# Kernel tuning notes

Hardware: AMD Instinct MI355X
Metric: run time of the kernel (lower is better)

## Reference

```python
import jax, jax.numpy as jnp
import numpy as np

N, E, D_IN, D_H, G = 20000, 320000, 512, 256, 128


def setup_inputs() -> dict:
    key = jax.random.key(0)
    ks = jax.random.split(key, 9)
    x = jax.random.normal(ks[0], (N, D_IN), dtype=jnp.float32)
    edge_index = jax.random.randint(ks[1], (2, E), 0, N, dtype=jnp.int32)
    batch = jnp.sort(jax.random.randint(ks[2], (N,), 0, G, dtype=jnp.int32))
    W1 = jax.random.normal(ks[3], (D_IN, D_H), dtype=jnp.float32) / np.float32(np.sqrt(D_IN))
    b1 = jnp.zeros((D_H,), dtype=jnp.float32)
    W2 = jax.random.normal(ks[4], (D_H, D_H), dtype=jnp.float32) / np.float32(np.sqrt(D_H))
    b2 = jnp.zeros((D_H,), dtype=jnp.float32)
    w_fc = jax.random.normal(ks[5], (D_H, 1), dtype=jnp.float32) / np.float32(np.sqrt(D_H))
    b_fc = jnp.zeros((1,), dtype=jnp.float32)
    return {"x": x, "edge_index": edge_index, "batch": batch,
            "W1": W1, "b1": b1, "W2": W2, "b2": b2, "w_fc": w_fc, "b_fc": b_fc}


def gcn_conv(x, W, b, src, dst, n):
    # PyG GCNConv: out = D^{-1/2} (A+I) D^{-1/2} (X W) + b  (self-loops already in src/dst)
    xw = x @ W                                            # [n, d_out]
    deg = jnp.zeros((n,), xw.dtype).at[dst].add(1.0)       # in-degree incl. self loop
    dinv = jnp.where(deg > 0, jax.lax.rsqrt(deg), 0.0)
    coef = (dinv[src] * dinv[dst])[:, None]               # [e, 1]
    out = jnp.zeros_like(xw).at[dst].add(xw[src] * coef)  # gather-scale-scatter
    return out + b


def reference(x, edge_index, batch, W1, b1, W2, b2, w_fc, b_fc):
    n = x.shape[0]
    loops = jnp.arange(n, dtype=edge_index.dtype)
    src = jnp.concatenate([edge_index[0], loops])
    dst = jnp.concatenate([edge_index[1], loops])
    h = jax.nn.relu(gcn_conv(x, W1, b1, src, dst, n))
    h = jax.nn.relu(gcn_conv(h, W2, b2, src, dst, n))
    # global_mean_pool over graph ids
    sums = jax.ops.segment_sum(h, batch, num_segments=G)                      # [G, d]
    cnt = jax.ops.segment_sum(jnp.ones((n, 1), h.dtype), batch, num_segments=G)
    pooled = sums / jnp.maximum(cnt, 1.0)
    return (pooled @ w_fc + b_fc)[:, 0]                                       # [G]
```

## Files before the change

kernel.cpp:

```cpp
#include <hip/hip_runtime.h>
#include <hip/hip_fp16.h>


#define TPB 256
#define CAP 64

typedef _Float16 hfrag __attribute__((ext_vector_type(8)));
typedef float f32x4 __attribute__((ext_vector_type(4)));
typedef float f32x2 __attribute__((ext_vector_type(2)));

__global__ __launch_bounds__(TPB) void k_init(int* __restrict__ cursor, int N,
                                              const float* __restrict__ W1,
                                              unsigned short* __restrict__ B1, int K1) {
  int nbz = (N + TPB - 1) / TPB;
  int b = blockIdx.x;
  if (b < nbz) {
    int i = b * TPB + threadIdx.x;
    if (i < N) cursor[i] = 0;
    return;
  }
  int t = (b - nbz) * TPB + threadIdx.x;
  if (t >= K1 * 256) return;
  int n = t & 255, k = t >> 8;
  __half h = __float2half(W1[(size_t)k * 256 + n]);
  B1[((size_t)(k >> 5) * 256 + n) * 32 + (k & 31)] = *(unsigned short*)&h;
}

#define LDSTR 72

template <int MODE>
__device__ __forceinline__ void gemm_core(const unsigned short* __restrict__ Bp,
                                          unsigned char* __restrict__ C, int M, int K,
                                          int bm, int bn,
                                          unsigned short (*As)[LDSTR],
                                          const float* A_f32,
                                          const __half* A_f16) {
  const int tid = threadIdx.x;
  const int w = tid >> 6;
  const int lane = tid & 63;
  const int q = lane >> 4;
  const int nin = lane & 15;
  const int r  = tid >> 3;
  const int cb = (tid & 7) << 3;
  const int row = bm + r;
  const bool rok = row < M;

  size_t bbase[2];
#pragma unroll
  for (int nt = 0; nt < 2; ++nt)
    bbase[nt] = ((size_t)(bn + w * 32 + nt * 16 + nin)) * 32 + q * 8;

  f32x4 acc[2][2];
#pragma unroll
  for (int mf = 0; mf < 2; ++mf)
#pragma unroll
    for (int nt = 0; nt < 2; ++nt) acc[mf][nt] = (f32x4){0.f, 0.f, 0.f, 0.f};

  float4 fA[2], fB[2];
  uint4  hA, hB;

  auto loadf = [&](float4* rf, int kb2) {
    const float* Ap = A_f32 + (size_t)row * K + kb2 + cb;
    rf[0] = *(const float4*)(Ap);
    rf[1] = *(const float4*)(Ap + 4);
  };
  auto loadh = [&](uint4& rh, int kb2) {
    rh = *(const uint4*)(A_f16 + (size_t)row * K + kb2 + cb);
  };
  auto stagef = [&](float4* rf) {
    float vv[8];
    *(float4*)&vv[0] = rf[0]; *(float4*)&vv[4] = rf[1];
    unsigned short h8[8];
#pragma unroll
    for (int j = 0; j < 8; ++j) {
      __half h = __float2half(vv[j]);
      h8[j] = *(unsigned short*)&h;
    }
    __syncthreads();
    *(uint4*)&As[r][cb] = *(uint4*)&h8[0];
    __syncthreads();
  };
  auto stageh = [&](uint4& rh) {
    __syncthreads();
    *(uint4*)&As[r][cb] = rh;
    __syncthreads();
  };
  auto mfma_step = [&](int kb2) {
#pragma unroll
    for (int s = 0; s < 2; ++s) {
      const size_t koff = (size_t)((kb2 >> 5) + s) * 256 * 32;
      hfrag bf[2];
#pragma unroll
      for (int nt = 0; nt < 2; ++nt)
        bf[nt] = *(const hfrag*)(Bp + koff + bbase[nt]);
      hfrag af[2];
#pragma unroll
      for (int mf = 0; mf < 2; ++mf)
        af[mf] = *(const hfrag*)&As[mf * 16 + nin][s * 32 + q * 8];
#pragma unroll
      for (int mf = 0; mf < 2; ++mf)
#pragma unroll
        for (int nt = 0; nt < 2; ++nt)
          acc[mf][nt] = __builtin_amdgcn_mfma_f32_16x16x32_f16(af[mf], bf[nt], acc[mf][nt], 0, 0, 0);
    }
  };

  if (MODE == 0) {
    fA[0] = make_float4(0.f, 0.f, 0.f, 0.f); fA[1] = fA[0];
    fB[0] = fA[0]; fB[1] = fA[0];
    if (rok) { loadf(fA, 0); loadf(fB, 64); }
  } else {
    hA = make_uint4(0, 0, 0, 0); hB = hA;
    if (rok) { loadh(hA, 0); loadh(hB, 64); }
  }

  for (int kb = 0; kb < K; kb += 128) {
    if (MODE == 0) stagef(fA); else stageh(hA);
    int kpA = kb + 128;
    if (kpA < K && rok) { if (MODE == 0) loadf(fA, kpA); else loadh(hA, kpA); }
    mfma_step(kb);
    if (MODE == 0) stagef(fB); else stageh(hB);
    int kpB = kb + 192;
    if (kpB < K && rok) { if (MODE == 0) loadf(fB, kpB); else loadh(hB, kpB); }
    mfma_step(kb + 64);
  }

#pragma unroll
  for (int mf = 0; mf < 2; ++mf) {
    int rb = bm + mf * 16 + q * 4;
#pragma unroll
    for (int reg = 0; reg < 4; ++reg) {
      int rr = rb + reg;
      if (rr < M) {
#pragma unroll
        for (int nt = 0; nt < 2; ++nt) {
          float v = acc[mf][nt][reg];
          int pk = __builtin_amdgcn_cvt_pk_fp8_f32(v, v, 0, false);
          C[(size_t)rr * 256 + bn + w * 32 + nt * 16 + nin] = (unsigned char)(pk & 0xff);
        }
      }
    }
  }
}

__global__ __launch_bounds__(TPB) void k_gemm1_scatter(const float* __restrict__ A,
                                                       const unsigned short* __restrict__ Bp,
                                                       unsigned char* __restrict__ C, int M, int K,
                                                       const int* __restrict__ src,
                                                       const int* __restrict__ dst,
                                                       int* __restrict__ cursor,
                                                       unsigned* __restrict__ pairw, int E,
                                                       const float* __restrict__ W2,
                                                       unsigned short* __restrict__ W2h) {
  __shared__ unsigned short As[32][LDSTR];
  int nbg = 2 * ((M + 31) / 32);
  int b = blockIdx.x;
  if (b < nbg) {
    gemm_core<0>(Bp, C, M, K, (b >> 1) * 32, (b & 1) * 128, As, A, nullptr);
    return;
  }
  b -= nbg;
  int nbE = (E + TPB - 1) / TPB;
  if (b < nbE) {
    int e = b * TPB + threadIdx.x;
    if (e >= E) return;
    int s = src[e], d = dst[e];
    int pos = d * CAP + atomicAdd(&cursor[d], 1);
    pairw[pos] = (unsigned)s;
    return;
  }
  b -= nbE;
  int t = b * TPB + threadIdx.x;
  if (t >= 256 * 256) return;
  int n = t & 255, k = t >> 8;
  __half h = __float2half(W2[(size_t)k * 256 + n]);
  W2h[((size_t)(k >> 5) * 256 + n) * 32 + (k & 31)] = *(unsigned short*)&h;
}

__global__ __launch_bounds__(TPB) void k_gemm2(const __half* __restrict__ A,
                                               const unsigned short* __restrict__ Bp,
                                               unsigned char* __restrict__ C, int M, int K) {
  __shared__ unsigned short As[32][LDSTR];
  gemm_core<1>(Bp, C, M, K, blockIdx.y * 32, blockIdx.x * 128, As, nullptr, A);
}

__device__ __forceinline__ void fma16(float* a, float coef, uint4 v) {
#pragma unroll
  for (int wv = 0; wv < 4; ++wv) {
    unsigned word = (&v.x)[wv];
    f32x2 lo = __builtin_amdgcn_cvt_pk_f32_fp8((int)word, false);
    f32x2 hi = __builtin_amdgcn_cvt_pk_f32_fp8((int)word, true);
    a[4 * wv + 0] = fmaf(coef, lo[0], a[4 * wv + 0]);
    a[4 * wv + 1] = fmaf(coef, lo[1], a[4 * wv + 1]);
    a[4 * wv + 2] = fmaf(coef, hi[0], a[4 * wv + 2]);
    a[4 * wv + 3] = fmaf(coef, hi[1], a[4 * wv + 3]);
  }
}

__device__ __forceinline__ void gather_loop(float* a, const uint4* __restrict__ xq,
                                            unsigned wreg, int deg, int quarter, int li) {
  int iters = (deg + 3) >> 2;
  int itersP = (iters + 3) & ~3;
  for (int p = 0; p < itersP; p += 4) {
    int k0 = 4 * p + quarter;
    unsigned w0 = (unsigned)__shfl((int)wreg, k0);
    unsigned w1 = (unsigned)__shfl((int)wreg, k0 + 4);
    unsigned w2 = (unsigned)__shfl((int)wreg, k0 + 8);
    unsigned w3 = (unsigned)__shfl((int)wreg, k0 + 12);
    uint4 v0 = xq[((size_t)(w0 >> 16) << 4) + li];
    uint4 v1 = xq[((size_t)(w1 >> 16) << 4) + li];
    uint4 v2 = xq[((size_t)(w2 >> 16) << 4) + li];
    uint4 v3 = xq[((size_t)(w3 >> 16) << 4) + li];
    unsigned short c0 = (unsigned short)(w0 & 0xFFFFu);
    unsigned short c1 = (unsigned short)(w1 & 0xFFFFu);
    unsigned short c2 = (unsigned short)(w2 & 0xFFFFu);
    unsigned short c3 = (unsigned short)(w3 & 0xFFFFu);
    fma16(a, __half2float(*(__half*)&c0), v0);
    fma16(a, __half2float(*(__half*)&c1), v1);
    fma16(a, __half2float(*(__half*)&c2), v2);
    fma16(a, __half2float(*(__half*)&c3), v3);
  }
#pragma unroll
  for (int i = 0; i < 16; ++i) a[i] += __shfl_xor(a[i], 16);
#pragma unroll
  for (int i = 0; i < 16; ++i) a[i] += __shfl_xor(a[i], 32);
}

__global__ __launch_bounds__(TPB) void k_gather1(const uint4* __restrict__ xq,
                                                 const int* __restrict__ cnt,
                                                 unsigned* __restrict__ pairw,
                                                 const float* __restrict__ bias,
                                                 uint4* __restrict__ h1, int N) {
  int node = __builtin_amdgcn_readfirstlane(blockIdx.x * 4 + (threadIdx.x >> 6));
  if (node >= N) return;
  int deg = __builtin_amdgcn_readfirstlane(cnt[node]);
  int lane = threadIdx.x & 63;
  int quarter = lane >> 4, li = lane & 15;
  int base = node * CAP;
  float ci = (float)(deg + 1);

  unsigned wreg = 0u;
  if (lane < deg) {
    int j = (int)pairw[base + lane];
    float c = rsqrtf(ci * (float)(cnt[j] + 1));
    __half hc = __float2half(c);
    wreg = ((unsigned)j << 16) | (unsigned)(*(unsigned short*)&hc);
    pairw[base + lane] = wreg;
  }

  float a[16];
#pragma unroll
  for (int i = 0; i < 16; ++i) a[i] = 0.f;
  gather_loop(a, xq, wreg, deg, quarter, li);

  float di2 = 1.f / ci;
  fma16(a, di2, xq[((size_t)node << 4) + li]);
  if (quarter == 0) {
    const float4 b0 = *(const float4*)&bias[16 * li];
    const float4 b1v = *(const float4*)&bias[16 * li + 4];
    const float4 b2v = *(const float4*)&bias[16 * li + 8];
    const float4 b3v = *(const float4*)&bias[16 * li + 12];
    float r[16];
    r[0] = fmaxf(a[0] + b0.x, 0.f);  r[1] = fmaxf(a[1] + b0.y, 0.f);
    r[2] = fmaxf(a[2] + b0.z, 0.f);  r[3] = fmaxf(a[3] + b0.w, 0.f);
    r[4] = fmaxf(a[4] + b1v.x, 0.f); r[5] = fmaxf(a[5] + b1v.y, 0.f);
    r[6] = fmaxf(a[6] + b1v.z, 0.f); r[7] = fmaxf(a[7] + b1v.w, 0.f);
    r[8] = fmaxf(a[8] + b2v.x, 0.f); r[9] = fmaxf(a[9] + b2v.y, 0.f);
    r[10] = fmaxf(a[10] + b2v.z, 0.f); r[11] = fmaxf(a[11] + b2v.w, 0.f);
    r[12] = fmaxf(a[12] + b3v.x, 0.f); r[13] = fmaxf(a[13] + b3v.y, 0.f);
    r[14] = fmaxf(a[14] + b3v.z, 0.f); r[15] = fmaxf(a[15] + b3v.w, 0.f);
    unsigned o[8];
#pragma unroll
    for (int i = 0; i < 8; ++i) {
      __half2 h2 = __floats2half2_rn(r[2 * i], r[2 * i + 1]);
      o[i] = *(unsigned*)&h2;
    }
    uint4 o0 = make_uint4(o[0], o[1], o[2], o[3]);
    uint4 o1 = make_uint4(o[4], o[5], o[6], o[7]);
    h1[(size_t)node * 32 + 2 * li] = o0;
    h1[(size_t)node * 32 + 2 * li + 1] = o1;
  }
}

__global__ __launch_bounds__(TPB) void k_gather2(const uint4* __restrict__ xq,
                                                 const int* __restrict__ cnt,
                                                 const unsigned* __restrict__ pairw,
                                                 const float* __restrict__ bias,
                                                 const float* __restrict__ wfc,
                                                 float* __restrict__ pdot, int N) {
  int node = __builtin_amdgcn_readfirstlane(blockIdx.x * 4 + (threadIdx.x >> 6));
  if (node >= N) return;
  int deg = __builtin_amdgcn_readfirstlane(cnt[node]);
  int lane = threadIdx.x & 63;
  int quarter = lane >> 4, li = lane & 15;
  int base = node * CAP;

  unsigned wreg = (lane < deg) ? pairw[base + lane] : 0u;

  float a[16];
#pragma unroll
  for (int i = 0; i < 16; ++i) a[i] = 0.f;
  gather_loop(a, xq, wreg, deg, quarter, li);

  float di2 = 1.f / (float)(deg + 1);
  fma16(a, di2, xq[((size_t)node << 4) + li]);

  const float4 b0 = *(const float4*)&bias[16 * li];
  const float4 b1v = *(const float4*)&bias[16 * li + 4];
  const float4 b2v = *(const float4*)&bias[16 * li + 8];
  const float4 b3v = *(const float4*)&bias[16 * li + 12];
  const float4 f0 = *(const float4*)&wfc[16 * li];
  const float4 f1 = *(const float4*)&wfc[16 * li + 4];
  const float4 f2 = *(const float4*)&wfc[16 * li + 8];
  const float4 f3 = *(const float4*)&wfc[16 * li + 12];
  float s = fmaxf(a[0] + b0.x, 0.f) * f0.x + fmaxf(a[1] + b0.y, 0.f) * f0.y +
            fmaxf(a[2] + b0.z, 0.f) * f0.z + fmaxf(a[3] + b0.w, 0.f) * f0.w +
            fmaxf(a[4] + b1v.x, 0.f) * f1.x + fmaxf(a[5] + b1v.y, 0.f) * f1.y +
            fmaxf(a[6] + b1v.z, 0.f) * f1.z + fmaxf(a[7] + b1v.w, 0.f) * f1.w +
            fmaxf(a[8] + b2v.x, 0.f) * f2.x + fmaxf(a[9] + b2v.y, 0.f) * f2.y +
            fmaxf(a[10] + b2v.z, 0.f) * f2.z + fmaxf(a[11] + b2v.w, 0.f) * f2.w +
            fmaxf(a[12] + b3v.x, 0.f) * f3.x + fmaxf(a[13] + b3v.y, 0.f) * f3.y +
            fmaxf(a[14] + b3v.z, 0.f) * f3.z + fmaxf(a[15] + b3v.w, 0.f) * f3.w;
#pragma unroll
  for (int off = 8; off > 0; off >>= 1) s += __shfl_down(s, off, 16);
  if (lane == 0) pdot[node] = s;
}

__global__ __launch_bounds__(TPB) void k_pool(const float* __restrict__ pdot,
                                              const int* __restrict__ batch,
                                              const float* __restrict__ bfc,
                                              float* __restrict__ out, int N) {
  int g = blockIdx.x;
  int lo = 0, hi = N;
  while (lo < hi) { int mid = (lo + hi) >> 1; if (batch[mid] < g) lo = mid + 1; else hi = mid; }
  int start = lo;
  hi = N;
  while (lo < hi) { int mid = (lo + hi) >> 1; if (batch[mid] < g + 1) lo = mid + 1; else hi = mid; }
  int end = lo;

  float s = 0.f;
  for (int i = start + threadIdx.x; i < end; i += TPB) s += pdot[i];
  __shared__ float red[4];
  int lane = threadIdx.x & 63, wave = threadIdx.x >> 6;
#pragma unroll
  for (int off = 32; off > 0; off >>= 1) s += __shfl_down(s, off);
  if (lane == 0) red[wave] = s;
  __syncthreads();
  if (threadIdx.x == 0) {
    float tot = red[0] + red[1] + red[2] + red[3];
    float c = (float)(end - start);
    out[g] = tot / fmaxf(c, 1.f) + bfc[0];
  }
}

extern "C" void kernel_launch(void* const* d_in, const int* in_sizes, int n_in,
                              void* d_out, int out_size, void* d_ws, size_t ws_size,
                              hipStream_t stream) {
  const float* x    = (const float*)d_in[0];
  const int*   eidx = (const int*)d_in[1];
  const int*   batch= (const int*)d_in[2];
  const float* W1   = (const float*)d_in[3];
  const float* b1   = (const float*)d_in[4];
  const float* W2   = (const float*)d_in[5];
  const float* b2   = (const float*)d_in[6];
  const float* wfc  = (const float*)d_in[7];
  const float* bfc  = (const float*)d_in[8];
  float* out = (float*)d_out;

  const int N  = in_sizes[2];
  const int E  = in_sizes[1] / 2;
  const int K1 = in_sizes[0] / N;
  const int G  = out_size;

  const int* srcp = eidx;
  const int* dstp = eidx + E;

  auto al16 = [](size_t v) { return (v + 15) & ~(size_t)15; };
  char* ws = (char*)d_ws;
  size_t off = 0;
  int*      cursor = (int*)(ws + off);         off = al16(off + (size_t)N * 4);
  unsigned* pairw  = (unsigned*)(ws + off);    off = al16(off + (size_t)N * CAP * 4);
  float*    pdot   = (float*)(ws + off);       off = al16(off + (size_t)N * 4);
  unsigned char* bufQ = (unsigned char*)(ws + off); off = al16(off + (size_t)N * 256);
  __half*   h1f    = (__half*)(ws + off);      off = al16(off + (size_t)N * 256 * 2);
  unsigned short* W1h = (unsigned short*)(ws + off); off = al16(off + (size_t)K1 * 256 * 2);
  unsigned short* W2h = (unsigned short*)(ws + off); off = al16(off + (size_t)256 * 256 * 2);

  const int nbz  = (N + TPB - 1) / TPB;
  const int nbW1 = (K1 * 256 + TPB - 1) / TPB;
  const int nbW2 = (256 * 256 + TPB - 1) / TPB;
  const int nbE  = (E + TPB - 1) / TPB;
  const int nbg  = 2 * ((N + 31) / 32);
  const int nbG  = (N + 3) / 4;
  const dim3 g2(2, (N + 31) / 32);

  k_init<<<nbz + nbW1, TPB, 0, stream>>>(cursor, N, W1, W1h, K1);

  k_gemm1_scatter<<<nbg + nbE + nbW2, TPB, 0, stream>>>(x, W1h, bufQ, N, K1,
                                                        srcp, dstp, cursor, pairw, E,
                                                        W2, W2h);
  k_gather1<<<nbG, TPB, 0, stream>>>((const uint4*)bufQ, cursor, pairw, b1,
                                     (uint4*)h1f, N);

  k_gemm2<<<g2, TPB, 0, stream>>>(h1f, W2h, bufQ, N, 256);

  k_gather2<<<nbG, TPB, 0, stream>>>((const uint4*)bufQ, cursor, pairw, b2,
                                     wfc, pdot, N);

  k_pool<<<G, TPB, 0, stream>>>(pdot, batch, bfc, out, N);
}
```

Before: 168.0 us.

## Use persistent grid-stride gather kernels with next-node prefetch, cap scatter blocks

Both gather kernels become persistent, with a capped grid of 1280 blocks looping over node groups. Each iteration prefetches the next node's degree and neighbour list while the current node is gathered, to hide load latency and cut block launch overhead. The edge-scatter part of the first GEMM kernel now uses a fixed 512 blocks with a grid-stride loop instead of one block per 256 edges. Risks are higher register pressure from the prefetch registers, and lower parallelism or tail imbalance when degrees vary.

```diff
diff --git a/kernel.cpp b/kernel.cpp
--- a/kernel.cpp
+++ b/kernel.cpp
@@ -4,6 +4,8 @@
 
 #define TPB 256
 #define CAP 64
+#define GBLK 1280
+#define SBLK 512
 
 typedef _Float16 hfrag __attribute__((ext_vector_type(8)));
 typedef float f32x4 __attribute__((ext_vector_type(4)));
@@ -160,16 +162,15 @@
     return;
   }
   b -= nbg;
-  int nbE = (E + TPB - 1) / TPB;
-  if (b < nbE) {
-    int e = b * TPB + threadIdx.x;
-    if (e >= E) return;
-    int s = src[e], d = dst[e];
-    int pos = d * CAP + atomicAdd(&cursor[d], 1);
-    pairw[pos] = (unsigned)s;
+  if (b < SBLK) {
+    for (int e = b * TPB + threadIdx.x; e < E; e += SBLK * TPB) {
+      int s = src[e], d = dst[e];
+      int pos = d * CAP + atomicAdd(&cursor[d], 1);
+      pairw[pos] = (unsigned)s;
+    }
     return;
   }
-  b -= nbE;
+  b -= SBLK;
   int t = b * TPB + threadIdx.x;
   if (t >= 256 * 256) return;
   int n = t & 255, k = t >> 8;
@@ -230,55 +231,79 @@
                                                  const int* __restrict__ cnt,
                                                  unsigned* __restrict__ pairw,
                                                  const float* __restrict__ bias,
-                                                 uint4* __restrict__ h1, int N) {
-  int node = __builtin_amdgcn_readfirstlane(blockIdx.x * 4 + (threadIdx.x >> 6));
-  if (node >= N) return;
-  int deg = __builtin_amdgcn_readfirstlane(cnt[node]);
-  int lane = threadIdx.x & 63;
-  int quarter = lane >> 4, li = lane & 15;
-  int base = node * CAP;
-  float ci = (float)(deg + 1);
-
-  unsigned wreg = 0u;
-  if (lane < deg) {
-    int j = (int)pairw[base + lane];
-    float c = rsqrtf(ci * (float)(cnt[j] + 1));
-    __half hc = __float2half(c);
-    wreg = ((unsigned)j << 16) | (unsigned)(*(unsigned short*)&hc);
-    pairw[base + lane] = wreg;
-  }
-
-  float a[16];
-#pragma unroll
-  for (int i = 0; i < 16; ++i) a[i] = 0.f;
-  gather_loop(a, xq, wreg, deg, quarter, li);
-
-  float di2 = 1.f / ci;
-  fma16(a, di2, xq[((size_t)node << 4) + li]);
-  if (quarter == 0) {
-    const float4 b0 = *(const float4*)&bias[16 * li];
-    const float4 b1v = *(const float4*)&bias[16 * li + 4];
-    const float4 b2v = *(const float4*)&bias[16 * li + 8];
-    const float4 b3v = *(const float4*)&bias[16 * li + 12];
-    float r[16];
-    r[0] = fmaxf(a[0] + b0.x, 0.f);  r[1] = fmaxf(a[1] + b0.y, 0.f);
-    r[2] = fmaxf(a[2] + b0.z, 0.f);  r[3] = fmaxf(a[3] + b0.w, 0.f);
-    r[4] = fmaxf(a[4] + b1v.x, 0.f); r[5] = fmaxf(a[5] + b1v.y, 0.f);
-    r[6] = fmaxf(a[6] + b1v.z, 0.f); r[7] = fmaxf(a[7] + b1v.w, 0.f);
-    r[8] = fmaxf(a[8] + b2v.x, 0.f); r[9] = fmaxf(a[9] + b2v.y, 0.f);
-    r[10] = fmaxf(a[10] + b2v.z, 0.f); r[11] = fmaxf(a[11] + b2v.w, 0.f);
-    r[12] = fmaxf(a[12] + b3v.x, 0.f); r[13] = fmaxf(a[13] + b3v.y, 0.f);
-    r[14] = fmaxf(a[14] + b3v.z, 0.f); r[15] = fmaxf(a[15] + b3v.w, 0.f);
-    unsigned o[8];
-#pragma unroll
-    for (int i = 0; i < 8; ++i) {
-      __half2 h2 = __floats2half2_rn(r[2 * i], r[2 * i + 1]);
-      o[i] = *(unsigned*)&h2;
-    }
-    uint4 o0 = make_uint4(o[0], o[1], o[2], o[3]);
-    uint4 o1 = make_uint4(o[4], o[5], o[6], o[7]);
-    h1[(size_t)node * 32 + 2 * li] = o0;
-    h1[(size_t)node * 32 + 2 * li + 1] = o1;
+                                                 uint4* __restrict__ h1, int N,
+                                                 int nblocks) {
+  const int lane = threadIdx.x & 63;
+  const int wv = threadIdx.x >> 6;
+  const int quarter = lane >> 4, li = lane & 15;
+  const int nwork = (N + 3) >> 2;
+
+  int g = blockIdx.x;
+  if (g >= nwork) return;
+  int node = g * 4 + wv;
+  bool nok = node < N;
+  int degS = nok ? cnt[node] : 0;
+  unsigned raw = nok ? pairw[(size_t)node * CAP + lane] : 0u;
+
+  for (;;) {
+    const int gn = g + nblocks;
+    const int nodeN = gn * 4 + wv;
+    const bool haveN = (gn < nwork) && (nodeN < N);
+
+    const int deg = __builtin_amdgcn_readfirstlane(degS);
+    const float ci = (float)(deg + 1);
+    const bool valid = nok && (lane < deg);
+    int j = valid ? (int)raw : 0;
+    int cj = valid ? cnt[j] : 0;
+
+    int degS_n = haveN ? cnt[nodeN] : 0;
+    unsigned raw_n = haveN ? pairw[(size_t)nodeN * CAP + lane] : 0u;
+
+    unsigned wreg = 0u;
+    if (valid) {
+      float c = rsqrtf(ci * (float)(cj + 1));
+      __half hc = __float2half(c);
+      wreg = ((unsigned)j << 16) | (unsigned)(*(unsigned short*)&hc);
+      pairw[(size_t)node * CAP + lane] = wreg;
+    }
+
+    if (nok) {
+      float a[16];
+#pragma unroll
+      for (int i = 0; i < 16; ++i) a[i] = 0.f;
+      gather_loop(a, xq, wreg, deg, quarter, li);
+
+      float di2 = 1.f / ci;
+      fma16(a, di2, xq[((size_t)node << 4) + li]);
+      if (quarter == 0) {
+        const float4 b0 = *(const float4*)&bias[16 * li];
+        const float4 b1v = *(const float4*)&bias[16 * li + 4];
+        const float4 b2v = *(const float4*)&bias[16 * li + 8];
+        const float4 b3v = *(const float4*)&bias[16 * li + 12];
+        float r[16];
+        r[0] = fmaxf(a[0] + b0.x, 0.f);  r[1] = fmaxf(a[1] + b0.y, 0.f);
+        r[2] = fmaxf(a[2] + b0.z, 0.f);  r[3] = fmaxf(a[3] + b0.w, 0.f);
+        r[4] = fmaxf(a[4] + b1v.x, 0.f); r[5] = fmaxf(a[5] + b1v.y, 0.f);
+        r[6] = fmaxf(a[6] + b1v.z, 0.f); r[7] = fmaxf(a[7] + b1v.w, 0.f);
+        r[8] = fmaxf(a[8] + b2v.x, 0.f); r[9] = fmaxf(a[9] + b2v.y, 0.f);
+        r[10] = fmaxf(a[10] + b2v.z, 0.f); r[11] = fmaxf(a[11] + b2v.w, 0.f);
+        r[12] = fmaxf(a[12] + b3v.x, 0.f); r[13] = fmaxf(a[13] + b3v.y, 0.f);
+        r[14] = fmaxf(a[14] + b3v.z, 0.f); r[15] = fmaxf(a[15] + b3v.w, 0.f);
+        unsigned o[8];
+#pragma unroll
+        for (int i = 0; i < 8; ++i) {
+          __half2 h2 = __floats2half2_rn(r[2 * i], r[2 * i + 1]);
+          o[i] = *(unsigned*)&h2;
+        }
+        uint4 o0 = make_uint4(o[0], o[1], o[2], o[3]);
+        uint4 o1 = make_uint4(o[4], o[5], o[6], o[7]);
+        h1[(size_t)node * 32 + 2 * li] = o0;
+        h1[(size_t)node * 32 + 2 * li + 1] = o1;
+      }
+    }
+
+    if (gn >= nwork) break;
+    g = gn; node = nodeN; nok = nodeN < N; degS = degS_n; raw = raw_n;
   }
 }
 
@@ -287,43 +312,65 @@
                                                  const unsigned* __restrict__ pairw,
                                                  const float* __restrict__ bias,
                                                  const float* __restrict__ wfc,
-                                                 float* __restrict__ pdot, int N) {
-  int node = __builtin_amdgcn_readfirstlane(blockIdx.x * 4 + (threadIdx.x >> 6));
-  if (node >= N) return;
-  int deg = __builtin_amdgcn_readfirstlane(cnt[node]);
-  int lane = threadIdx.x & 63;
-  int quarter = lane >> 4, li = lane & 15;
-  int base = node * CAP;
-
-  unsigned wreg = (lane < deg) ? pairw[base + lane] : 0u;
-
-  float a[16];
-#pragma unroll
-  for (int i = 0; i < 16; ++i) a[i] = 0.f;
-  gather_loop(a, xq, wreg, deg, quarter, li);
-
-  float di2 = 1.f / (float)(deg + 1);
-  fma16(a, di2, xq[((size_t)node << 4) + li]);
-
-  const float4 b0 = *(const float4*)&bias[16 * li];
-  const float4 b1v = *(const float4*)&bias[16 * li + 4];
-  const float4 b2v = *(const float4*)&bias[16 * li + 8];
-  const float4 b3v = *(const float4*)&bias[16 * li + 12];
-  const float4 f0 = *(const float4*)&wfc[16 * li];
-  const float4 f1 = *(const float4*)&wfc[16 * li + 4];
-  const float4 f2 = *(const float4*)&wfc[16 * li + 8];
-  const float4 f3 = *(const float4*)&wfc[16 * li + 12];
-  float s = fmaxf(a[0] + b0.x, 0.f) * f0.x + fmaxf(a[1] + b0.y, 0.f) * f0.y +
-            fmaxf(a[2] + b0.z, 0.f) * f0.z + fmaxf(a[3] + b0.w, 0.f) * f0.w +
-            fmaxf(a[4] + b1v.x, 0.f) * f1.x + fmaxf(a[5] + b1v.y, 0.f) * f1.y +
-            fmaxf(a[6] + b1v.z, 0.f) * f1.z + fmaxf(a[7] + b1v.w, 0.f) * f1.w +
-            fmaxf(a[8] + b2v.x, 0.f) * f2.x + fmaxf(a[9] + b2v.y, 0.f) * f2.y +
-            fmaxf(a[10] + b2v.z, 0.f) * f2.z + fmaxf(a[11] + b2v.w, 0.f) * f2.w +
-            fmaxf(a[12] + b3v.x, 0.f) * f3.x + fmaxf(a[13] + b3v.y, 0.f) * f3.y +
-            fmaxf(a[14] + b3v.z, 0.f) * f3.z + fmaxf(a[15] + b3v.w, 0.f) * f3.w;
-#pragma unroll
-  for (int off = 8; off > 0; off >>= 1) s += __shfl_down(s, off, 16);
-  if (lane == 0) pdot[node] = s;
+                                                 float* __restrict__ pdot, int N,
+                                                 int nblocks) {
+  const int lane = threadIdx.x & 63;
+  const int wv = threadIdx.x >> 6;
+  const int quarter = lane >> 4, li = lane & 15;
+  const int nwork = (N + 3) >> 2;
+
+  int g = blockIdx.x;
+  if (g >= nwork) return;
+  int node = g * 4 + wv;
+  bool nok = node < N;
+  int degS = nok ? cnt[node] : 0;
+  unsigned raw = nok ? pairw[(size_t)node * CAP + lane] : 0u;
+
+  for (;;) {
+    const int gn = g + nblocks;
+    const int nodeN = gn * 4 + wv;
+    const bool haveN = (gn < nwork) && (nodeN < N);
+
+    const int deg = __builtin_amdgcn_readfirstlane(degS);
+    const bool valid = nok && (lane < deg);
+    const unsigned wreg = valid ? raw : 0u;
+
+    int degS_n = haveN ? cnt[nodeN] : 0;
+    unsigned raw_n = haveN ? pairw[(size_t)nodeN * CAP + lane] : 0u;
+
+    if (nok) {
+      float a[16];
+#pragma unroll
+      for (int i = 0; i < 16; ++i) a[i] = 0.f;
+      gather_loop(a, xq, wreg, deg, quarter, li);
+
+      float di2 = 1.f / (float)(deg + 1);
+      fma16(a, di2, xq[((size_t)node << 4) + li]);
+
+      const float4 b0 = *(const float4*)&bias[16 * li];
+      const float4 b1v = *(const float4*)&bias[16 * li + 4];
+      const float4 b2v = *(const float4*)&bias[16 * li + 8];
+      const float4 b3v = *(const float4*)&bias[16 * li + 12];
+      const float4 f0 = *(const float4*)&wfc[16 * li];
+      const float4 f1 = *(const float4*)&wfc[16 * li + 4];
+      const float4 f2 = *(const float4*)&wfc[16 * li + 8];
+      const float4 f3 = *(const float4*)&wfc[16 * li + 12];
+      float s = fmaxf(a[0] + b0.x, 0.f) * f0.x + fmaxf(a[1] + b0.y, 0.f) * f0.y +
+                fmaxf(a[2] + b0.z, 0.f) * f0.z + fmaxf(a[3] + b0.w, 0.f) * f0.w +
+                fmaxf(a[4] + b1v.x, 0.f) * f1.x + fmaxf(a[5] + b1v.y, 0.f) * f1.y +
+                fmaxf(a[6] + b1v.z, 0.f) * f1.z + fmaxf(a[7] + b1v.w, 0.f) * f1.w +
+                fmaxf(a[8] + b2v.x, 0.f) * f2.x + fmaxf(a[9] + b2v.y, 0.f) * f2.y +
+                fmaxf(a[10] + b2v.z, 0.f) * f2.z + fmaxf(a[11] + b2v.w, 0.f) * f2.w +
+                fmaxf(a[12] + b3v.x, 0.f) * f3.x + fmaxf(a[13] + b3v.y, 0.f) * f3.y +
+                fmaxf(a[14] + b3v.z, 0.f) * f3.z + fmaxf(a[15] + b3v.w, 0.f) * f3.w;
+#pragma unroll
+      for (int off = 8; off > 0; off >>= 1) s += __shfl_down(s, off, 16);
+      if (lane == 0) pdot[node] = s;
+    }
+
+    if (gn >= nwork) break;
+    g = gn; node = nodeN; nok = nodeN < N; degS = degS_n; raw = raw_n;
+  }
 }
 
 __global__ __launch_bounds__(TPB) void k_pool(const float* __restrict__ pdot,
@@ -389,23 +436,23 @@
   const int nbz  = (N + TPB - 1) / TPB;
   const int nbW1 = (K1 * 256 + TPB - 1) / TPB;
   const int nbW2 = (256 * 256 + TPB - 1) / TPB;
-  const int nbE  = (E + TPB - 1) / TPB;
   const int nbg  = 2 * ((N + 31) / 32);
-  const int nbG  = (N + 3) / 4;
+  const int nwork = (N + 3) / 4;
+  const int nbG  = nwork < GBLK ? nwork : GBLK;
   const dim3 g2(2, (N + 31) / 32);
 
   k_init<<<nbz + nbW1, TPB, 0, stream>>>(cursor, N, W1, W1h, K1);
 
-  k_gemm1_scatter<<<nbg + nbE + nbW2, TPB, 0, stream>>>(x, W1h, bufQ, N, K1,
-                                                        srcp, dstp, cursor, pairw, E,
-                                                        W2, W2h);
+  k_gemm1_scatter<<<nbg + SBLK + nbW2, TPB, 0, stream>>>(x, W1h, bufQ, N, K1,
+                                                         srcp, dstp, cursor, pairw, E,
+                                                         W2, W2h);
   k_gather1<<<nbG, TPB, 0, stream>>>((const uint4*)bufQ, cursor, pairw, b1,
-                                     (uint4*)h1f, N);
+                                     (uint4*)h1f, N, nbG);
 
   k_gemm2<<<g2, TPB, 0, stream>>>(h1f, W2h, bufQ, N, 256);
 
   k_gather2<<<nbG, TPB, 0, stream>>>((const uint4*)bufQ, cursor, pairw, b2,
-                                     wfc, pdot, N);
+                                     wfc, pdot, N, nbG);
 
   k_pool<<<G, TPB, 0, stream>>>(pdot, batch, bfc, out, N);
 }
```

Result: slower. 178.2 us (+6.1%).
